# Kernel optimization log

Measured on AMD Instinct MI355X. Metric: run time of the kernel, lower is better.

The kernel has to match this reference:

```python
import jax, jax.numpy as jnp
import numpy as np

HEADS, DIM_HEAD, LANDMARKS, PINV_ITERS, CONV_K = 8, 64, 256, 6, 33


def iter_pinv(x, iters=PINV_ITERS):
    # Moore-Penrose iterative pseudo-inverse (lucidrains nystrom_attention)
    abs_x = jnp.abs(x)
    scale = abs_x.sum(-1).max() * abs_x.sum(-2).max()  # global maxes, as in torch.max
    z = jnp.swapaxes(x, -1, -2) / scale
    I = jnp.eye(x.shape[-1], dtype=x.dtype)
    for _ in range(iters):
        xz = x @ z
        z = 0.25 * z @ (13.0 * I - xz @ (15.0 * I - xz @ (7.0 * I - xz)))
    return z


def nystrom_attention(h, W_qkv, W_out, b_out, conv_w):
    b, n, _ = h.shape
    inner = HEADS * DIM_HEAD
    qkv = h @ W_qkv  # (b, n, 3*inner), bias=False
    q, k, v = jnp.split(qkv, 3, axis=-1)
    split_heads = lambda t: t.reshape(b, n, HEADS, DIM_HEAD).transpose(0, 2, 1, 3)
    q, k, v = split_heads(q), split_heads(k), split_heads(v)  # (b,h,n,dh)
    q = q * (DIM_HEAD ** -0.5)
    l = n // LANDMARKS  # tokens per landmark (n divisible by m, so no padding)
    q_l = q.reshape(b, HEADS, LANDMARKS, l, DIM_HEAD).mean(3)
    k_l = k.reshape(b, HEADS, LANDMARKS, l, DIM_HEAD).mean(3)
    sim1 = jnp.einsum('bhnd,bhmd->bhnm', q, k_l)      # (b,h,n,m)
    sim2 = jnp.einsum('bhmd,bhld->bhml', q_l, k_l)    # (b,h,m,m)
    sim3 = jnp.einsum('bhmd,bhnd->bhmn', q_l, k)      # (b,h,m,n)
    attn1 = jax.nn.softmax(sim1, -1)
    attn2 = jax.nn.softmax(sim2, -1)
    attn3 = jax.nn.softmax(sim3, -1)
    out = (attn1 @ iter_pinv(attn2)) @ (attn3 @ v)    # (b,h,n,dh)
    # residual depthwise conv along sequence dim: Conv2d(heads, heads, (33,1), groups=heads, no bias)
    res = jax.lax.conv_general_dilated(
        v, conv_w, window_strides=(1, 1),
        padding=((CONV_K // 2, CONV_K // 2), (0, 0)),
        feature_group_count=HEADS)
    out = out + res
    out = out.transpose(0, 2, 1, 3).reshape(b, n, inner)
    return out @ W_out + b_out


def setup_inputs() -> dict:
    key = jax.random.key(0)
    ks = jax.random.split(key, 8)
    N, Din, Dout = 8192, 1024, 256
    inner = HEADS * DIM_HEAD
    s = 0.02
    return {
        'x': jax.random.normal(ks[0], (1, N, Din), jnp.float32),
        'W_ft': jax.random.normal(ks[1], (Din, Dout), jnp.float32) * s,
        'b_ft': jnp.zeros((Dout,), jnp.float32),
        'W_qkv': jax.random.normal(ks[2], (Dout, 3 * inner), jnp.float32) * s,
        'W_out': jax.random.normal(ks[3], (inner, Dout), jnp.float32) * s,
        'b_out': jnp.zeros((Dout,), jnp.float32),
        'conv_w': jax.random.normal(ks[4], (HEADS, 1, CONV_K, 1), jnp.float32) * s,
        'W_score': jax.random.normal(ks[5], (Dout, 1), jnp.float32) * s,
        'b_score': jnp.zeros((1,), jnp.float32),
    }


def reference(x, W_ft, b_ft, W_qkv, W_out, b_out, conv_w, W_score, b_score):
    # feature_transform: Linear -> Dropout (identity in eval) -> ReLU
    h = jax.nn.relu(x @ W_ft + b_ft)                 # (1, N, Dout)
    af = nystrom_attention(h, W_qkv, W_out, b_out, conv_w)
    # score_layer: Linear -> Dropout -> ReLU
    scores = jax.nn.relu(af @ W_score + b_score)     # (1, N, 1)
    scores = scores[0].T                             # (1, N)
    weights = jax.nn.softmax(scores, axis=1)         # (1, N)
    aggregated = weights @ h[0]                      # (1, Dout)
    return aggregated, weights
```

## Files before the change

### kernel.cpp

```cpp
#include <hip/hip_runtime.h>

typedef unsigned short u16;
typedef __attribute__((ext_vector_type(8))) short s16x8;
typedef __attribute__((ext_vector_type(4))) float f32x4;
typedef __attribute__((ext_vector_type(8))) unsigned short u16x8;

__device__ inline float b2f(u16 u) {
  unsigned x = ((unsigned)u) << 16;
  return __builtin_bit_cast(float, x);
}
__device__ inline u16 f2b(float f) {
  unsigned u = __builtin_bit_cast(unsigned, f);
  u += 0x7fffu + ((u >> 16) & 1u);
  return (u16)(u >> 16);
}

#define GLL(src, dst) __builtin_amdgcn_global_load_lds( \
    (const __attribute__((address_space(1))) unsigned int*)(src), \
    (__attribute__((address_space(3))) unsigned int*)(dst), 16, 0, 0)

struct MP {
  const u16* A; const u16* B;
  u16* C; u16* Ct; float* Cf; u16* vTo;
  const u16* Aadd; const float* bias;
  const float* Ws; float* sc;
  int M, N, K;
  int lda, ldb, ldc, ldct, ldcf, ldaadd;
  long long bA, bB, bC, bCt, bCf, bAadd;
  float alpha, beta;
  int relu, scale_cols; float colscale;
  int kchunks;
};

template<int BM, int BN, bool F32A>
__global__ __launch_bounds__(256) void gemm_mfma(MP p)
{
  constexpr int WM = BM / 2, WN = BN / 2;
  constexpr int FM = WM / 16, FN = WN / 16;
  constexpr int APAN = BM / 16, BPAN = BN / 16, NPAN = APAN + BPAN;
  constexpr int APW = (APAN + 3) / 4;
  __shared__ __align__(16) u16 lds[2 * NPAN * 512];

  const int tid = threadIdx.x, lane = tid & 63, wid = tid >> 6;
  const int bz = blockIdx.z;
  const int batch = (p.kchunks > 1) ? bz / p.kchunks : bz;
  const int kc    = (p.kchunks > 1) ? bz % p.kchunks : 0;
  const u16* A = p.A + (long long)batch * p.bA + (long long)kc * p.K;
  const float* Af32 = (const float*)p.A + (long long)batch * p.bA + (long long)kc * p.K;
  const u16* B = p.B + (long long)batch * p.bB + (long long)kc * p.K;
  const int m0 = blockIdx.y * BM, n0 = blockIdx.x * BN;
  const int srow = lane & 15, skoff = (lane >> 4) * 8;
  const int wm0 = (wid >> 1) * WM, wn0 = (wid & 1) * WN;

  f32x4 acc[FM][FN];
#pragma unroll
  for (int i = 0; i < FM; i++)
#pragma unroll
    for (int j = 0; j < FN; j++) acc[i][j] = (f32x4){0.f, 0.f, 0.f, 0.f};

  float4 areg[APW][2];

  auto stage_all = [&](int sb, int kt) {
#pragma unroll
    for (int pp = wid; pp < NPAN; pp += 4) {
      const u16* src = (pp < APAN)
        ? A + (size_t)(m0 + pp * 16 + srow) * p.lda + kt + skoff
        : B + (size_t)(n0 + (pp - APAN) * 16 + srow) * p.ldb + kt + skoff;
      GLL(src, &lds[sb * (NPAN * 512) + pp * 512]);
    }
  };
  auto stage_b = [&](int sb, int kt) {
#pragma unroll
    for (int pp = APAN + wid; pp < NPAN; pp += 4) {
      const u16* src = B + (size_t)(n0 + (pp - APAN) * 16 + srow) * p.ldb + kt + skoff;
      GLL(src, &lds[sb * (NPAN * 512) + pp * 512]);
    }
  };
  auto load_a = [&](int kt) {
#pragma unroll
    for (int ap = 0; ap < APW; ap++) {
      int pp = wid + ap * 4;
      const float* src = Af32 + (size_t)(m0 + pp * 16 + srow) * p.lda + kt + skoff;
      areg[ap][0] = ((const float4*)src)[0];
      areg[ap][1] = ((const float4*)src)[1];
    }
  };
  auto write_a = [&](int sb) {
#pragma unroll
    for (int ap = 0; ap < APW; ap++) {
      int pp = wid + ap * 4;
      u16 t[8];
      t[0] = f2b(areg[ap][0].x); t[1] = f2b(areg[ap][0].y);
      t[2] = f2b(areg[ap][0].z); t[3] = f2b(areg[ap][0].w);
      t[4] = f2b(areg[ap][1].x); t[5] = f2b(areg[ap][1].y);
      t[6] = f2b(areg[ap][1].z); t[7] = f2b(areg[ap][1].w);
      *(s16x8*)&lds[sb * (NPAN * 512) + pp * 512 + lane * 8] = *(const s16x8*)t;
    }
  };
  auto compute = [&](int sb) {
    const int bo = sb * (NPAN * 512);
    s16x8 afr[FM], bfr[FN];
#pragma unroll
    for (int i = 0; i < FM; i++)
      afr[i] = *(const s16x8*)&lds[bo + (wm0 / 16 + i) * 512 + lane * 8];
#pragma unroll
    for (int j = 0; j < FN; j++)
      bfr[j] = *(const s16x8*)&lds[bo + (APAN + wn0 / 16 + j) * 512 + lane * 8];
#pragma unroll
    for (int i = 0; i < FM; i++)
#pragma unroll
      for (int j = 0; j < FN; j++)
        acc[i][j] = __builtin_amdgcn_mfma_f32_16x16x32_bf16(afr[i], bfr[j], acc[i][j], 0, 0, 0);
  };

  const int nt = p.K / 32;
  int buf = 0;
  if constexpr (F32A) { load_a(0); stage_b(0, 0); write_a(0); }
  else                { stage_all(0, 0); }
  asm volatile("s_waitcnt vmcnt(0)" ::: "memory");
  __syncthreads();

  for (int t = 0; t < nt; ++t) {
    if constexpr (F32A) {
      if (t + 1 < nt) { load_a((t + 1) * 32); stage_b(buf ^ 1, (t + 1) * 32); }
      compute(buf);
      if (t + 1 < nt) write_a(buf ^ 1);
    } else {
      if (t + 1 < nt) stage_all(buf ^ 1, (t + 1) * 32);
      compute(buf);
    }
    asm volatile("s_waitcnt vmcnt(0)" ::: "memory");
    __syncthreads();
    buf ^= 1;
  }

  const int r0 = (lane >> 4) * 4, c0 = lane & 15;

  if (p.Ws) {
    float* sb = (float*)lds;
#pragma unroll
    for (int i = 0; i < FM; i++)
#pragma unroll
      for (int q = 0; q < 4; q++) {
        float s = 0.f;
#pragma unroll
        for (int j = 0; j < FN; j++)
          s += acc[i][j][q] * p.Ws[wn0 + j * 16 + c0];
        s += __shfl_xor(s, 1); s += __shfl_xor(s, 2);
        s += __shfl_xor(s, 4); s += __shfl_xor(s, 8);
        if ((lane & 15) == 0) sb[(wid & 1) * 64 + wm0 + i * 16 + r0 + q] = s;
      }
    __syncthreads();
    if (tid < 64)
      p.sc[(size_t)bz * 8192 + m0 + tid] = sb[tid] + sb[64 + tid];
    return;
  }

#pragma unroll
  for (int i = 0; i < FM; i++) {
#pragma unroll
    for (int j = 0; j < FN; j++) {
#pragma unroll
      for (int q = 0; q < 4; q++) {
        const int gr = m0 + wm0 + i * 16 + r0 + q;
        const int gc = n0 + wn0 + j * 16 + c0;
        float c = p.alpha * acc[i][j][q];
        if (p.Aadd) c += p.beta * b2f(p.Aadd[(long long)batch * p.bAadd + (size_t)gr * p.ldaadd + gc]);
        if (p.bias) c += p.bias[gc];
        if (gc < p.scale_cols) c *= p.colscale;
        if (p.relu) c = fmaxf(c, 0.f);
        if (p.Cf) p.Cf[(long long)bz * p.bCf + (size_t)gr * p.ldcf + gc] = c;
        u16 b = f2b(c);
        if (p.C)  p.C [(long long)batch * p.bC + (size_t)gr * p.ldc + gc] = b;
        if (p.Ct) p.Ct[(long long)batch * p.bCt + (size_t)gc * p.ldct + gr] = b;
        if (p.vTo && gc >= 1024) p.vTo[(size_t)(gc - 1024) * 8192 + gr] = b;
      }
    }
  }
}

__global__ void reduce_bias_bf16(const float* __restrict__ parts,
                                 const float* __restrict__ bias,
                                 u16* __restrict__ out)
{
  const int i4 = blockIdx.x * 256 + threadIdx.x;
  float4 s = ((const float4*)parts)[i4];
#pragma unroll
  for (int k = 1; k < 4; k++) {
    float4 v = ((const float4*)parts)[(size_t)k * 524288 + i4];
    s.x += v.x; s.y += v.y; s.z += v.z; s.w += v.w;
  }
  const float4 b = ((const float4*)bias)[i4 & 63];
  s.x = fmaxf(s.x + b.x, 0.f); s.y = fmaxf(s.y + b.y, 0.f);
  s.z = fmaxf(s.z + b.z, 0.f); s.w = fmaxf(s.w + b.w, 0.f);
  ushort4 o; o.x = f2b(s.x); o.y = f2b(s.y); o.z = f2b(s.z); o.w = f2b(s.w);
  ((ushort4*)out)[i4] = o;
}

struct AVF { const u16 *qkvb, *ql, *vT; float *Cf, *den; };

__global__ __launch_bounds__(256) void av_fused(AVF p)
{
  __shared__ __align__(16) u16 lds[20480];
  const int tid = threadIdx.x, lane = tid & 63, wid = tid >> 6;
  const int bz = blockIdx.z, head = bz >> 4, kc = bz & 15;
  const int m0 = blockIdx.y * 128;
  const int srow = lane & 15, skoff = (lane >> 4) * 8;
  const int r0 = (lane >> 4) * 4, c0 = lane & 15;
  const u16* Kb = p.qkvb + 512 + (size_t)(kc * 512) * 1536 + head * 64;
  const u16* Vb = p.vT + (size_t)head * 524288 + kc * 512;
  const u16* QL = p.ql + head * 16384 + (size_t)m0 * 64;

#pragma unroll
  for (int q = 0; q < 4; q++) {
    int pid = wid * 4 + q, pr = pid >> 1, kc2 = pid & 1;
    GLL(QL + (size_t)(pr * 16 + srow) * 64 + kc2 * 32 + skoff, &lds[pid * 512]);
  }
  auto stage_kv = [&](int sb, int t) {
    int kr = wid >> 1, kc2 = wid & 1;
    GLL(Kb + (size_t)(t * 32 + kr * 16 + srow) * 1536 + kc2 * 32 + skoff,
        &lds[8192 + sb * 2048 + wid * 512]);
    GLL(Vb + (size_t)(wid * 16 + srow) * 8192 + t * 32 + skoff,
        &lds[12288 + sb * 2048 + wid * 512]);
  };

  f32x4 acc[4][2];
#pragma unroll
  for (int i = 0; i < 4; i++)
#pragma unroll
    for (int j = 0; j < 2; j++) acc[i][j] = (f32x4){0.f, 0.f, 0.f, 0.f};
  float den[2][4];
#pragma unroll
  for (int i = 0; i < 2; i++)
#pragma unroll
    for (int q = 0; q < 4; q++) den[i][q] = 0.f;

  const int nt = 16;
  int buf = 0;
  stage_kv(0, 0);
  asm volatile("s_waitcnt vmcnt(0)" ::: "memory");
  __syncthreads();

  for (int t = 0; t < nt; ++t) {
    if (t + 1 < nt) stage_kv(buf ^ 1, t + 1);
    f32x4 s[2][2];
#pragma unroll
    for (int i = 0; i < 2; i++)
#pragma unroll
      for (int j = 0; j < 2; j++) s[i][j] = (f32x4){0.f, 0.f, 0.f, 0.f};
#pragma unroll
    for (int t2 = 0; t2 < 2; t2++) {
      s16x8 aq[2], bk[2];
#pragma unroll
      for (int i = 0; i < 2; i++)
        aq[i] = *(const s16x8*)&lds[((wid * 2 + i) * 2 + t2) * 512 + lane * 8];
#pragma unroll
      for (int j = 0; j < 2; j++)
        bk[j] = *(const s16x8*)&lds[8192 + buf * 2048 + (j * 2 + t2) * 512 + lane * 8];
#pragma unroll
      for (int i = 0; i < 2; i++)
#pragma unroll
        for (int j = 0; j < 2; j++)
          s[i][j] = __builtin_amdgcn_mfma_f32_16x16x32_bf16(aq[i], bk[j], s[i][j], 0, 0, 0);
    }
#pragma unroll
    for (int i = 0; i < 2; i++)
#pragma unroll
      for (int j = 0; j < 2; j++)
#pragma unroll
        for (int q = 0; q < 4; q++) {
          float e = expf(s[i][j][q]);
          den[i][q] += e;
          int kk = j * 16 + c0;
          lds[16384 + (wid * 2 + i) * 512 + (r0 + q) * 8 + (kk >> 3) * 128 + (kk & 7)] = f2b(e);
        }
    asm volatile("s_waitcnt vmcnt(0)" ::: "memory");
    __syncthreads();
    {
      s16x8 afr[4], bfr[2];
#pragma unroll
      for (int i = 0; i < 4; i++)
        afr[i] = *(const s16x8*)&lds[16384 + ((wid >> 1) * 4 + i) * 512 + lane * 8];
#pragma unroll
      for (int j = 0; j < 2; j++)
        bfr[j] = *(const s16x8*)&lds[12288 + buf * 2048 + ((wid & 1) * 2 + j) * 512 + lane * 8];
#pragma unroll
      for (int i = 0; i < 4; i++)
#pragma unroll
        for (int j = 0; j < 2; j++)
          acc[i][j] = __builtin_amdgcn_mfma_f32_16x16x32_bf16(afr[i], bfr[j], acc[i][j], 0, 0, 0);
    }
    __syncthreads();
    buf ^= 1;
  }

#pragma unroll
  for (int i = 0; i < 4; i++)
#pragma unroll
    for (int j = 0; j < 2; j++)
#pragma unroll
      for (int q = 0; q < 4; q++) {
        const int gr = m0 + (wid >> 1) * 64 + i * 16 + r0 + q;
        const int gc = (wid & 1) * 32 + j * 16 + c0;
        p.Cf[(size_t)bz * 16384 + (size_t)gr * 64 + gc] = acc[i][j][q];
      }
#pragma unroll
  for (int i = 0; i < 2; i++)
#pragma unroll
    for (int q = 0; q < 4; q++) {
      float v = den[i][q];
      v += __shfl_xor(v, 1); v += __shfl_xor(v, 2);
      v += __shfl_xor(v, 4); v += __shfl_xor(v, 8);
      if (c0 == 0)
        p.den[(size_t)bz * 256 + m0 + wid * 32 + i * 16 + r0 + q] = v;
    }
}

struct FA1 { const u16 *qkvb, *kl, *MmT; u16 *af; };

__global__ __launch_bounds__(256) void fused_attn1(FA1 p)
{
  __shared__ __align__(16) u16 lds[36864];
  __shared__ float mb[4][64];
  const int tid = threadIdx.x, lane = tid & 63, wid = tid >> 6;
  const int head = blockIdx.y, n0 = blockIdx.x * 64;
  const int srow = lane & 15, skoff = (lane >> 4) * 8;
  const int rbase = (lane >> 4) * 4;

  for (int pid = wid; pid < 72; pid += 4) {
    const u16* src;
    if (pid < 8) {
      int pr = pid >> 1, kc = pid & 1;
      src = p.qkvb + (size_t)(n0 + pr * 16 + srow) * 1536 + head * 64 + kc * 32 + skoff;
    } else if (pid < 40) {
      int j = pid - 8, pr = j >> 1, kc = j & 1;
      src = p.kl + head * 16384 + (size_t)(pr * 16 + srow) * 64 + kc * 32 + skoff;
    } else {
      int j = pid - 40, pr = j >> 3, kc = j & 7;
      src = p.MmT + head * 16384 + (size_t)(pr * 16 + srow) * 256 + kc * 32 + skoff;
    }
    GLL(src, &lds[pid * 512]);
  }
  asm volatile("s_waitcnt vmcnt(0)" ::: "memory");
  __syncthreads();

  const int wr = (wid >> 1) * 32, ch_ = wid & 1;
  f32x4 s[2][8];
#pragma unroll
  for (int i = 0; i < 2; i++)
#pragma unroll
    for (int j = 0; j < 8; j++) s[i][j] = (f32x4){0.f, 0.f, 0.f, 0.f};
#pragma unroll
  for (int t = 0; t < 2; t++) {
    s16x8 a[2], b[8];
#pragma unroll
    for (int i = 0; i < 2; i++)
      a[i] = *(const s16x8*)&lds[(((wid >> 1) * 2 + i) * 2 + t) * 512 + lane * 8];
#pragma unroll
    for (int j = 0; j < 8; j++)
      b[j] = *(const s16x8*)&lds[4096 + ((ch_ * 8 + j) * 2 + t) * 512 + lane * 8];
#pragma unroll
    for (int i = 0; i < 2; i++)
#pragma unroll
      for (int j = 0; j < 8; j++)
        s[i][j] = __builtin_amdgcn_mfma_f32_16x16x32_bf16(a[i], b[j], s[i][j], 0, 0, 0);
  }
#pragma unroll
  for (int i = 0; i < 2; i++)
#pragma unroll
    for (int q = 0; q < 4; q++) {
      float rm = -INFINITY;
#pragma unroll
      for (int j = 0; j < 8; j++) rm = fmaxf(rm, s[i][j][q]);
#pragma unroll
      for (int off = 1; off < 16; off <<= 1) rm = fmaxf(rm, __shfl_xor(rm, off));
      if ((lane & 15) == 0) mb[ch_][wr + i * 16 + rbase + q] = rm;
    }
  __syncthreads();
  float m_[2][4];
#pragma unroll
  for (int i = 0; i < 2; i++)
#pragma unroll
    for (int q = 0; q < 4; q++)
      m_[i][q] = fmaxf(mb[0][wr + i * 16 + rbase + q], mb[1][wr + i * 16 + rbase + q]);
#pragma unroll
  for (int i = 0; i < 2; i++)
#pragma unroll
    for (int q = 0; q < 4; q++) {
      float ss = 0.f;
#pragma unroll
      for (int j = 0; j < 8; j++) {
        float e = expf(s[i][j][q] - m_[i][q]);
        s[i][j][q] = e; ss += e;
      }
#pragma unroll
      for (int off = 1; off < 16; off <<= 1) ss += __shfl_xor(ss, off);
      if ((lane & 15) == 0) mb[2 + ch_][wr + i * 16 + rbase + q] = ss;
    }
  __syncthreads();
#pragma unroll
  for (int i = 0; i < 2; i++)
#pragma unroll
    for (int q = 0; q < 4; q++) {
      int row = wr + i * 16 + rbase + q;
      float inv = 1.f / (mb[2][row] + mb[3][row]);
#pragma unroll
      for (int j = 0; j < 8; j++)
        lds[(size_t)row * 264 + ch_ * 128 + j * 16 + (lane & 15)] = f2b(s[i][j][q] * inv);
    }
  __syncthreads();
  const int wr2 = (wid >> 1) * 32, wd2 = (wid & 1) * 32;
  f32x4 acc[2][2];
#pragma unroll
  for (int i = 0; i < 2; i++)
#pragma unroll
    for (int jd = 0; jd < 2; jd++) acc[i][jd] = (f32x4){0.f, 0.f, 0.f, 0.f};
#pragma unroll
  for (int t = 0; t < 8; t++) {
    s16x8 a[2], b[2];
#pragma unroll
    for (int i = 0; i < 2; i++)
      a[i] = *(const s16x8*)&lds[(size_t)(wr2 + i * 16 + (lane & 15)) * 264 + t * 32 + (lane >> 4) * 8];
#pragma unroll
    for (int jd = 0; jd < 2; jd++)
      b[jd] = *(const s16x8*)&lds[20480 + (((wid & 1) * 2 + jd) * 8 + t) * 512 + lane * 8];
#pragma unroll
    for (int i = 0; i < 2; i++)
#pragma unroll
      for (int jd = 0; jd < 2; jd++)
        acc[i][jd] = __builtin_amdgcn_mfma_f32_16x16x32_bf16(a[i], b[jd], acc[i][jd], 0, 0, 0);
  }
#pragma unroll
  for (int i = 0; i < 2; i++)
#pragma unroll
    for (int jd = 0; jd < 2; jd++)
#pragma unroll
      for (int q = 0; q < 4; q++)
        p.af[(size_t)(n0 + wr2 + i * 16 + rbase + q) * 512 + head * 64 + wd2 + jd * 16 + (lane & 15)]
            = f2b(acc[i][jd][q]);
}

__global__ void conv_res_add_bf16(const u16* __restrict__ qkvb,
                                  const float* __restrict__ convw,
                                  u16* __restrict__ af)
{
  __shared__ float vt[96][64];
  const int h = blockIdx.y, n0 = blockIdx.x * 64;
  const int t = threadIdx.x, ch = t & 63, r0 = t >> 6;
  for (int r = r0; r < 96; r += 4) {
    int n = n0 - 16 + r;
    float v = 0.f;
    if (n >= 0 && n < 8192) v = b2f(qkvb[(size_t)n * 1536 + 1024 + h * 64 + ch]);
    vt[r][ch] = v;
  }
  __syncthreads();
  float w[33];
#pragma unroll
  for (int j = 0; j < 33; j++) w[j] = convw[h * 33 + j];
  for (int tl = r0; tl < 64; tl += 4) {
    float acc = 0.f;
#pragma unroll
    for (int j = 0; j < 33; j++) acc += w[j] * vt[tl + j][ch];
    size_t o = (size_t)(n0 + tl) * 512 + h * 64 + ch;
    af[o] = f2b(b2f(af[o]) + acc);
  }
}

__global__ void fused_tail(const float* __restrict__ sp,
                           const float* __restrict__ wconst,
                           const u16* __restrict__ hb, float* __restrict__ out)
{
  __shared__ float red[256];
  const int t = threadIdx.x, c = blockIdx.x;
  const float wc = wconst[0];
  float e[32];
  float m = -INFINITY;
#pragma unroll
  for (int i = 0; i < 32; i++) {
    int idx = t + i * 256;
    float v = sp[idx] + sp[8192 + idx] + sp[16384 + idx] + sp[24576 + idx] + wc;
    v = fmaxf(v, 0.f);
    e[i] = v; m = fmaxf(m, v);
  }
  red[t] = m; __syncthreads();
  for (int s = 128; s; s >>= 1) { if (t < s) red[t] = fmaxf(red[t], red[t + s]); __syncthreads(); }
  m = red[0]; __syncthreads();
  float ls = 0.f;
#pragma unroll
  for (int i = 0; i < 32; i++) { e[i] = expf(e[i] - m); ls += e[i]; }
  red[t] = ls; __syncthreads();
  for (int s = 128; s; s >>= 1) { if (t < s) red[t] += red[t + s]; __syncthreads(); }
  const float inv = 1.f / red[0];
  __syncthreads();

  if (c < 256) {
    float acc = 0.f;
#pragma unroll
    for (int i = 0; i < 32; i++)
      acc += e[i] * inv * b2f(hb[(size_t)(t + i * 256) * 256 + c]);
    red[t] = acc; __syncthreads();
    for (int s = 128; s; s >>= 1) { if (t < s) red[t] += red[t + s]; __syncthreads(); }
    if (t == 0) out[c] = red[0];
  } else {
#pragma unroll
    for (int i = 0; i < 32; i++) out[256 + t + i * 256] = e[i] * inv;
  }
}

__global__ void prescale(const u16* __restrict__ x2, float* __restrict__ sbuf)
{
  const int h = blockIdx.x, t = threadIdx.x;
  const u16* X = x2 + ((size_t)h << 16);
  float cs = 0.f;
  for (int r = 0; r < 256; r++) cs += fabsf(b2f(X[r * 256 + t]));
  float rs = 0.f;
  for (int c4 = 0; c4 < 256; c4 += 4) {
    ushort4 v = *(const ushort4*)(X + (size_t)t * 256 + c4);
    rs += fabsf(b2f(v.x)) + fabsf(b2f(v.y)) + fabsf(b2f(v.z)) + fabsf(b2f(v.w));
  }
  __shared__ float red[512];
  red[t] = rs; red[256 + t] = cs;
  __syncthreads();
  for (int s = 128; s; s >>= 1) {
    if (t < s) {
      red[t] = fmaxf(red[t], red[t + s]);
      red[256 + t] = fmaxf(red[256 + t], red[256 + t + s]);
    }
    __syncthreads();
  }
  if (t == 0) { sbuf[h] = red[0]; sbuf[8 + h] = red[256]; }
}

__global__ void pinv_init(const u16* __restrict__ x2, const float* __restrict__ sbuf,
                          u16* __restrict__ z0, u16* __restrict__ z0T)
{
  __shared__ u16 tile[64][80];
  const int t = threadIdx.x;
  const size_t base = (size_t)blockIdx.y << 16;
  const int tr = (blockIdx.x >> 2) * 64, tc = (blockIdx.x & 3) * 64;
  const u16* X = x2 + base;

  float mr = -INFINITY, mc = -INFINITY;
#pragma unroll
  for (int i = 0; i < 8; i++) {
    mr = fmaxf(mr, sbuf[i]);
    mc = fmaxf(mc, sbuf[8 + i]);
  }
  const float inv = 1.f / (mr * mc);

  {
    int r = t >> 2, cg = (t & 3) * 16;
#pragma unroll
    for (int v4 = 0; v4 < 4; v4++) {
      ushort4 v = *(const ushort4*)(X + (size_t)(tr + r) * 256 + tc + cg + v4 * 4);
      v.x = f2b(b2f(v.x) * inv); v.y = f2b(b2f(v.y) * inv);
      v.z = f2b(b2f(v.z) * inv); v.w = f2b(b2f(v.w) * inv);
      *(ushort4*)(z0T + base + (size_t)(tr + r) * 256 + tc + cg + v4 * 4) = v;
      *(ushort4*)&tile[r][cg + v4 * 4] = v;
    }
  }
  __syncthreads();
  {
    int c = t >> 2, rg = (t & 3) * 16;
    u16 o[16];
#pragma unroll
    for (int e = 0; e < 16; e++) o[e] = tile[rg + e][c];
#pragma unroll
    for (int v4 = 0; v4 < 4; v4++)
      *(ushort4*)(z0 + base + (size_t)(tc + c) * 256 + tr + rg + v4 * 4) = *(ushort4*)&o[v4 * 4];
  }
}

struct PG {
  const u16 *U, *V, *Xadd, *XaddT;
  u16 *DR, *DT;
  float alpha, beta;
};

template<bool WD, bool WDT>
__global__ __launch_bounds__(256) void pinv_gemm(PG p)
{
  __shared__ __align__(16) u16 lds[65536 / 2];
  const int tid = threadIdx.x, lane = tid & 63, wid = tid >> 6;
  const size_t base = (size_t)blockIdx.z << 16;
  const u16* U = p.U + base;
  const u16* V = p.V + base;
  const int m0 = blockIdx.y * 64, n0 = blockIdx.x * 64;
  const int srow = lane & 15, skoff = (lane >> 4) * 8;
  const int wr = (wid >> 1) * 32, wc = (wid & 1) * 32;

#pragma unroll
  for (int q = 0; q < 16; q++) {
    const int pid = wid * 16 + q;
    const int rg = (pid >> 3) & 3, t = pid & 7;
    const u16* src = (pid < 32)
      ? U + (size_t)(m0 + rg * 16 + srow) * 256 + t * 32 + skoff
      : V + (size_t)(n0 + rg * 16 + srow) * 256 + t * 32 + skoff;
    GLL(src, &lds[pid * 512]);
  }
  asm volatile("s_waitcnt vmcnt(0)" ::: "memory");
  __syncthreads();

  f32x4 acc[2][2], accT[2][2];
#pragma unroll
  for (int i = 0; i < 2; i++)
#pragma unroll
    for (int j = 0; j < 2; j++) {
      acc[i][j] = (f32x4){0.f, 0.f, 0.f, 0.f};
      accT[i][j] = (f32x4){0.f, 0.f, 0.f, 0.f};
    }

#pragma unroll
  for (int t = 0; t < 8; t++) {
    s16x8 afr[2], bfr[2];
#pragma unroll
    for (int i = 0; i < 2; i++)
      afr[i] = *(const s16x8*)&lds[((wr / 16 + i) * 8 + t) * 512 + lane * 8];
#pragma unroll
    for (int j = 0; j < 2; j++)
      bfr[j] = *(const s16x8*)&lds[(32 + (wc / 16 + j) * 8 + t) * 512 + lane * 8];
#pragma unroll
    for (int i = 0; i < 2; i++)
#pragma unroll
      for (int j = 0; j < 2; j++) {
        if constexpr (WD)
          acc[i][j] = __builtin_amdgcn_mfma_f32_16x16x32_bf16(afr[i], bfr[j], acc[i][j], 0, 0, 0);
        if constexpr (WDT)
          accT[j][i] = __builtin_amdgcn_mfma_f32_16x16x32_bf16(bfr[j], afr[i], accT[j][i], 0, 0, 0);
      }
  }

  const int r0 = (lane >> 4) * 4, c0 = lane & 15;
  if constexpr (WD) {
    const u16* Xa = p.Xadd ? p.Xadd + base : nullptr;
    u16* DR = p.DR + base;
#pragma unroll
    for (int i = 0; i < 2; i++)
#pragma unroll
      for (int j = 0; j < 2; j++)
#pragma unroll
        for (int q = 0; q < 4; q++) {
          const int gr = m0 + wr + i * 16 + r0 + q;
          const int gc = n0 + wc + j * 16 + c0;
          float v = p.alpha * acc[i][j][q];
          if (Xa) v += p.beta * b2f(Xa[(size_t)gr * 256 + gc]);
          DR[(size_t)gr * 256 + gc] = f2b(v);
        }
  }
  if constexpr (WDT) {
    const u16* Xt = p.XaddT ? p.XaddT + base : nullptr;
    u16* DT = p.DT + base;
#pragma unroll
    for (int j = 0; j < 2; j++)
#pragma unroll
      for (int i = 0; i < 2; i++)
#pragma unroll
        for (int q = 0; q < 4; q++) {
          const int gn = n0 + wc + j * 16 + r0 + q;
          const int gm = m0 + wr + i * 16 + c0;
          float v = p.alpha * accT[j][i][q];
          if (Xt) v += p.beta * b2f(Xt[(size_t)gn * 256 + gm]);
          DT[(size_t)gn * 256 + gm] = f2b(v);
        }
  }
}

struct PR1 { const u16 *A, *At, *z; u16 *B, *Bt, *G, *Gt, *W; };

__global__ __launch_bounds__(256) void pinv_r1(PR1 p)
{
  __shared__ __align__(16) u16 lds[32768];
  const int tid = threadIdx.x, lane = tid & 63, wid = tid >> 6;
  const int prob = blockIdx.z >> 3;
  const size_t base = (size_t)(blockIdx.z & 7) << 16;
  const u16* U = (prob ? p.z : p.A) + base;
  const u16* V = p.At + base;
  const int m0 = blockIdx.y * 64, n0 = blockIdx.x * 64;
  const int srow = lane & 15, skoff = (lane >> 4) * 8;
  const int wr = (wid >> 1) * 32, wc = (wid & 1) * 32;

#pragma unroll
  for (int q = 0; q < 16; q++) {
    const int pid = wid * 16 + q;
    const int rg = (pid >> 3) & 3, t = pid & 7;
    const u16* src = (pid < 32)
      ? U + (size_t)(m0 + rg * 16 + srow) * 256 + t * 32 + skoff
      : V + (size_t)(n0 + rg * 16 + srow) * 256 + t * 32 + skoff;
    GLL(src, &lds[pid * 512]);
  }
  asm volatile("s_waitcnt vmcnt(0)" ::: "memory");
  __syncthreads();

  f32x4 acc[2][2], accT[2][2];
#pragma unroll
  for (int i = 0; i < 2; i++)
#pragma unroll
    for (int j = 0; j < 2; j++) {
      acc[i][j] = (f32x4){0.f, 0.f, 0.f, 0.f};
      accT[i][j] = (f32x4){0.f, 0.f, 0.f, 0.f};
    }

#pragma unroll
  for (int t = 0; t < 8; t++) {
    s16x8 afr[2], bfr[2];
#pragma unroll
    for (int i = 0; i < 2; i++)
      afr[i] = *(const s16x8*)&lds[((wr / 16 + i) * 8 + t) * 512 + lane * 8];
#pragma unroll
    for (int j = 0; j < 2; j++)
      bfr[j] = *(const s16x8*)&lds[(32 + (wc / 16 + j) * 8 + t) * 512 + lane * 8];
#pragma unroll
    for (int i = 0; i < 2; i++)
#pragma unroll
      for (int j = 0; j < 2; j++) {
        acc[i][j] = __builtin_amdgcn_mfma_f32_16x16x32_bf16(afr[i], bfr[j], acc[i][j], 0, 0, 0);
        if (prob == 0)
          accT[j][i] = __builtin_amdgcn_mfma_f32_16x16x32_bf16(bfr[j], afr[i], accT[j][i], 0, 0, 0);
      }
  }

  const int r0 = (lane >> 4) * 4, c0 = lane & 15;
  if (prob == 0) {
    const u16* Ab  = p.A  + base;
    const u16* Atb = p.At + base;
    u16 *Bv = p.B + base, *Btv = p.Bt + base;
    u16 *Gv = p.G + base, *Gtv = p.Gt + base;
#pragma unroll
    for (int i = 0; i < 2; i++)
#pragma unroll
      for (int j = 0; j < 2; j++)
#pragma unroll
        for (int q = 0; q < 4; q++) {
          const int gr = m0 + wr + i * 16 + r0 + q;
          const int gc = n0 + wc + j * 16 + c0;
          float b = acc[i][j][q];
          float a = b2f(Ab[(size_t)gr * 256 + gc]);
          Bv[(size_t)gr * 256 + gc] = f2b(b);
          Gv[(size_t)gr * 256 + gc] = f2b(7.f * a - b);
        }
#pragma unroll
    for (int j = 0; j < 2; j++)
#pragma unroll
      for (int i = 0; i < 2; i++)
#pragma unroll
        for (int q = 0; q < 4; q++) {
          const int gn = n0 + wc + j * 16 + r0 + q;
          const int gm = m0 + wr + i * 16 + c0;
          float bt = accT[j][i][q];
          float at = b2f(Atb[(size_t)gn * 256 + gm]);
          Btv[(size_t)gn * 256 + gm] = f2b(bt);
          Gtv[(size_t)gn * 256 + gm] = f2b(7.f * at - bt);
        }
  } else {
    u16* Wv = p.W + base;
#pragma unroll
    for (int i = 0; i < 2; i++)
#pragma unroll
      for (int j = 0; j < 2; j++)
#pragma unroll
        for (int q = 0; q < 4; q++) {
          const int gr = m0 + wr + i * 16 + r0 + q;
          const int gc = n0 + wc + j * 16 + c0;
          Wv[(size_t)gr * 256 + gc] = f2b(acc[i][j][q]);
        }
  }
}

struct PR2 { const u16 *W, *G, *Gt, *B, *Bt, *z, *A, *At; u16 *zo, *Ao, *Aot; };

__global__ __launch_bounds__(256) void pinv_r2(PR2 p)
{
  __shared__ __align__(16) u16 lds[32768];
  const int tid = threadIdx.x, lane = tid & 63, wid = tid >> 6;
  const int prob = blockIdx.z >> 3;
  const size_t base = (size_t)(blockIdx.z & 7) << 16;
  const u16* U = (prob ? p.G  : p.W ) + base;
  const u16* V = (prob ? p.Bt : p.Gt) + base;
  const int m0 = blockIdx.y * 64, n0 = blockIdx.x * 64;
  const int srow = lane & 15, skoff = (lane >> 4) * 8;
  const int wr = (wid >> 1) * 32, wc = (wid & 1) * 32;

#pragma unroll
  for (int q = 0; q < 16; q++) {
    const int pid = wid * 16 + q;
    const int rg = (pid >> 3) & 3, t = pid & 7;
    const u16* src = (pid < 32)
      ? U + (size_t)(m0 + rg * 16 + srow) * 256 + t * 32 + skoff
      : V + (size_t)(n0 + rg * 16 + srow) * 256 + t * 32 + skoff;
    GLL(src, &lds[pid * 512]);
  }
  asm volatile("s_waitcnt vmcnt(0)" ::: "memory");
  __syncthreads();

  f32x4 acc[2][2], accT[2][2];
#pragma unroll
  for (int i = 0; i < 2; i++)
#pragma unroll
    for (int j = 0; j < 2; j++) {
      acc[i][j] = (f32x4){0.f, 0.f, 0.f, 0.f};
      accT[i][j] = (f32x4){0.f, 0.f, 0.f, 0.f};
    }

#pragma unroll
  for (int t = 0; t < 8; t++) {
    s16x8 afr[2], bfr[2];
#pragma unroll
    for (int i = 0; i < 2; i++)
      afr[i] = *(const s16x8*)&lds[((wr / 16 + i) * 8 + t) * 512 + lane * 8];
#pragma unroll
    for (int j = 0; j < 2; j++)
      bfr[j] = *(const s16x8*)&lds[(32 + (wc / 16 + j) * 8 + t) * 512 + lane * 8];
#pragma unroll
    for (int i = 0; i < 2; i++)
#pragma unroll
      for (int j = 0; j < 2; j++) {
        acc[i][j] = __builtin_amdgcn_mfma_f32_16x16x32_bf16(afr[i], bfr[j], acc[i][j], 0, 0, 0);
        if (prob)
          accT[j][i] = __builtin_amdgcn_mfma_f32_16x16x32_bf16(bfr[j], afr[i], accT[j][i], 0, 0, 0);
      }
  }

  const int r0 = (lane >> 4) * 4, c0 = lane & 15;
  if (prob == 0) {
    const u16* Zb = p.z + base;
    const u16* Wb = p.W + base;
    u16* Zo = p.zo + base;
#pragma unroll
    for (int i = 0; i < 2; i++)
#pragma unroll
      for (int j = 0; j < 2; j++)
#pragma unroll
        for (int q = 0; q < 4; q++) {
          const int gr = m0 + wr + i * 16 + r0 + q;
          const int gc = n0 + wc + j * 16 + c0;
          float v = 0.25f * acc[i][j][q]
                  + 3.25f * b2f(Zb[(size_t)gr * 256 + gc])
                  - 3.75f * b2f(Wb[(size_t)gr * 256 + gc]);
          Zo[(size_t)gr * 256 + gc] = f2b(v);
        }
  } else {
    const u16* Ab  = p.A  + base;
    const u16* Bb  = p.B  + base;
    const u16* Atb = p.At + base;
    const u16* Btb = p.Bt + base;
    u16* Ao  = p.Ao  + base;
    u16* Aot = p.Aot + base;
#pragma unroll
    for (int i = 0; i < 2; i++)
#pragma unroll
      for (int j = 0; j < 2; j++)
#pragma unroll
        for (int q = 0; q < 4; q++) {
          const int gr = m0 + wr + i * 16 + r0 + q;
          const int gc = n0 + wc + j * 16 + c0;
          float v = 0.25f * acc[i][j][q]
                  + 3.25f * b2f(Ab[(size_t)gr * 256 + gc])
                  - 3.75f * b2f(Bb[(size_t)gr * 256 + gc]);
          Ao[(size_t)gr * 256 + gc] = f2b(v);
        }
#pragma unroll
    for (int j = 0; j < 2; j++)
#pragma unroll
      for (int i = 0; i < 2; i++)
#pragma unroll
        for (int q = 0; q < 4; q++) {
          const int gn = n0 + wc + j * 16 + r0 + q;
          const int gm = m0 + wr + i * 16 + c0;
          float v = 0.25f * accT[j][i][q]
                  + 3.25f * b2f(Atb[(size_t)gn * 256 + gm])
                  - 3.75f * b2f(Btb[(size_t)gn * 256 + gm]);
          Aot[(size_t)gn * 256 + gm] = f2b(v);
        }
  }
}

__global__ void prep_weights(const float* __restrict__ Wft, const float* __restrict__ Wqkv,
                             const float* __restrict__ Wout, u16* __restrict__ WftT,
                             u16* __restrict__ WqkvT, u16* __restrict__ WoutT,
                             const float* __restrict__ bout, const float* __restrict__ Wsc,
                             const float* __restrict__ bsc, float* __restrict__ wconst)
{
  int idx = blockIdx.x * 256 + threadIdx.x;
  if (blockIdx.x == 0 && threadIdx.x < 64) {
    int c = threadIdx.x * 4;
    float s = bout[c] * Wsc[c] + bout[c + 1] * Wsc[c + 1]
            + bout[c + 2] * Wsc[c + 2] + bout[c + 3] * Wsc[c + 3];
    for (int off = 1; off < 64; off <<= 1) s += __shfl_xor(s, off);
    if (threadIdx.x == 0) wconst[0] = s + bsc[0];
  }
  if (idx < 262144) {
    int r = idx & 1023, c = idx >> 10;
    WftT[idx] = f2b(Wft[(size_t)r * 256 + c]);
  } else if (idx < 655360) {
    int i = idx - 262144;
    int r = i & 255, c = i >> 8;
    WqkvT[i] = f2b(Wqkv[(size_t)r * 1536 + c]);
  } else {
    int i = idx - 655360;
    int r = i & 511, c = i >> 9;
    WoutT[i] = f2b(Wout[(size_t)r * 256 + c]);
  }
}

__global__ void landmark_means(const u16* __restrict__ qkvb,
                               u16* __restrict__ ql, u16* __restrict__ kl)
{
  int idx = blockIdx.x * 256 + threadIdx.x;
  int which = idx >> 17, r = idx & 131071;
  int h = r >> 14, m = (r >> 6) & 255, d = r & 63;
  const u16* src = qkvb + (which ? 512 : 0) + h * 64 + d;
  float s = 0.f; int n0 = m * 32;
  for (int i = 0; i < 32; i++) s += b2f(src[(size_t)(n0 + i) * 1536]);
  (which ? kl : ql)[r] = f2b(s * (1.f / 32.f));
}

__global__ void softmax_rows_bf16_256(u16* __restrict__ d)
{
  const int row = blockIdx.x * 4 + (threadIdx.x >> 6);
  const int lane = threadIdx.x & 63;
  ushort4* p = (ushort4*)(d + (size_t)row * 256);
  ushort4 raw = p[lane];
  float v0 = b2f(raw.x), v1 = b2f(raw.y), v2 = b2f(raw.z), v3 = b2f(raw.w);
  float mx = fmaxf(fmaxf(v0, v1), fmaxf(v2, v3));
  for (int off = 1; off < 64; off <<= 1) mx = fmaxf(mx, __shfl_xor(mx, off));
  v0 = expf(v0 - mx); v1 = expf(v1 - mx); v2 = expf(v2 - mx); v3 = expf(v3 - mx);
  float s = v0 + v1 + v2 + v3;
  for (int off = 1; off < 64; off <<= 1) s += __shfl_xor(s, off);
  float inv = 1.f / s;
  raw.x = f2b(v0 * inv); raw.y = f2b(v1 * inv); raw.z = f2b(v2 * inv); raw.w = f2b(v3 * inv);
  p[lane] = raw;
}

__global__ void reduce_avT(const float* __restrict__ avp, const float* __restrict__ den,
                           u16* __restrict__ avT)
{
  int idx = blockIdx.x * 256 + threadIdx.x;
  int m = idx & 255, d = (idx >> 8) & 63, h = idx >> 14;
  float s = 0.f, l = 0.f;
  for (int c = 0; c < 16; c++) {
    s += avp[((size_t)(h * 16 + c)) * 16384 + m * 64 + d];
    l += den[(size_t)(h * 16 + c) * 256 + m];
  }
  avT[((size_t)h * 64 + d) * 256 + m] = f2b(s / l);
}

extern "C" void kernel_launch(void* const* d_in, const int* in_sizes, int n_in,
                              void* d_out, int out_size, void* d_ws, size_t ws_size,
                              hipStream_t stream)
{
  const float* x       = (const float*)d_in[0];
  const float* W_ft    = (const float*)d_in[1];
  const float* b_ft    = (const float*)d_in[2];
  const float* W_qkv   = (const float*)d_in[3];
  const float* W_out   = (const float*)d_in[4];
  const float* b_out   = (const float*)d_in[5];
  const float* conv_w  = (const float*)d_in[6];
  const float* W_score = (const float*)d_in[7];
  const float* b_score = (const float*)d_in[8];
  float* out = (float*)d_out;

  char* W = (char*)d_ws;
  auto alloc = [&](size_t bytes) { char* r = W; W += (bytes + 255) & ~(size_t)255; return r; };
  u16* WftT  = (u16*)alloc(256ull * 1024 * 2);
  u16* WqkvT = (u16*)alloc(1536ull * 256 * 2);
  u16* WoutT = (u16*)alloc(256ull * 512 * 2);
  u16* hb    = (u16*)alloc(8192ull * 256 * 2);
  u16* qkvb  = (u16*)alloc(8192ull * 1536 * 2);
  u16* ql    = (u16*)alloc(8ull * 256 * 64 * 2);
  u16* kl    = (u16*)alloc(8ull * 256 * 64 * 2);
  u16* x2    = (u16*)alloc(8ull * 256 * 256 * 2);
  u16* z0    = (u16*)alloc(8ull * 256 * 256 * 2);
  u16* z0T   = (u16*)alloc(8ull * 256 * 256 * 2);
  u16* zp    = (u16*)alloc(8ull * 256 * 256 * 2);
  u16* Amat  = (u16*)alloc(8ull * 256 * 256 * 2);
  u16* AmatT = (u16*)alloc(8ull * 256 * 256 * 2);
  u16* Am2   = (u16*)alloc(8ull * 256 * 256 * 2);
  u16* Am2T  = (u16*)alloc(8ull * 256 * 256 * 2);
  u16* Bm    = (u16*)alloc(8ull * 256 * 256 * 2);
  u16* BmT   = (u16*)alloc(8ull * 256 * 256 * 2);
  u16* Gm    = (u16*)alloc(8ull * 256 * 256 * 2);
  u16* GmT   = (u16*)alloc(8ull * 256 * 256 * 2);
  u16* Wm    = (u16*)alloc(8ull * 256 * 256 * 2);
  u16* vT    = (u16*)alloc(8ull * 64 * 8192 * 2);
  float* avp = (float*)alloc(8ull * 16 * 256 * 64 * 4);
  float* denp = (float*)alloc(128ull * 256 * 4);
  u16* avT   = (u16*)alloc(8ull * 64 * 256 * 2);
  u16* MmT   = (u16*)alloc(8ull * 64 * 256 * 2);
  u16* af    = (u16*)alloc(8192ull * 512 * 2);
  float* gpart = (float*)alloc(4ull * 8192 * 256 * 4);
  float* sbuf   = (float*)alloc(256);
  float* scores = (float*)alloc(4ull * 8192 * 4);
  float* wconst = (float*)alloc(256);

  auto mp = [](const u16* A, const u16* B, int M, int N, int K,
               int lda, int ldb, long long bA, long long bB) {
    MP p{}; p.A = A; p.B = B; p.M = M; p.N = N; p.K = K;
    p.lda = lda; p.ldb = ldb; p.bA = bA; p.bB = bB;
    p.alpha = 1.f; p.beta = 0.f; p.kchunks = 1; return p;
  };

  prep_weights<<<3072, 256, 0, stream>>>(W_ft, W_qkv, W_out, WftT, WqkvT, WoutT,
                                         b_out, W_score, b_score, wconst);

  { MP p = mp((const u16*)x, WftT, 8192, 256, 256, 1024, 1024, 0, 0);
    p.kchunks = 4; p.Cf = gpart; p.ldcf = 256; p.bCf = 2097152;
    gemm_mfma<64, 256, true><<<dim3(1, 128, 4), 256, 0, stream>>>(p); }
  reduce_bias_bf16<<<2048, 256, 0, stream>>>(gpart, b_ft, hb);

  { MP p = mp(hb, WqkvT, 8192, 1536, 256, 256, 256, 0, 0);
    p.C = qkvb; p.ldc = 1536; p.scale_cols = 512; p.colscale = 0.125f; p.vTo = vT;
    gemm_mfma<128, 128, false><<<dim3(12, 64, 1), 256, 0, stream>>>(p); }

  landmark_means<<<1024, 256, 0, stream>>>(qkvb, ql, kl);

  { MP p = mp(ql, kl, 256, 256, 64, 64, 64, 16384, 16384);
    p.C = x2; p.ldc = 256; p.bC = 65536;
    gemm_mfma<64, 64, false><<<dim3(4, 4, 8), 256, 0, stream>>>(p); }
  softmax_rows_bf16_256<<<512, 256, 0, stream>>>(x2);

  prescale<<<8, 256, 0, stream>>>(x2, sbuf);
  pinv_init<<<dim3(16, 8), 256, 0, stream>>>(x2, sbuf, z0, z0T);
  { PG p{x2, z0T, nullptr, nullptr, Amat, AmatT, 1.f, 0.f};
    pinv_gemm<true, true><<<dim3(4, 4, 8), 256, 0, stream>>>(p); }
  {
    const dim3 b(256);
    u16 *zr = z0, *zo = zp;
    u16 *Ar = Amat, *Art = AmatT, *Ao = Am2, *Aot = Am2T;
    for (int it = 0; it < 6; it++) {
      { PR1 r{Ar, Art, zr, Bm, BmT, Gm, GmT, Wm};
        pinv_r1<<<dim3(4, 4, 16), b, 0, stream>>>(r); }
      { PR2 r{Wm, Gm, GmT, Bm, BmT, zr, Ar, Art, zo, Ao, Aot};
        pinv_r2<<<dim3(4, 4, (it == 5) ? 8 : 16), b, 0, stream>>>(r); }
      u16* t;
      t = zr; zr = zo; zo = t;
      t = Ar; Ar = Ao; Ao = t;
      t = Art; Art = Aot; Aot = t;
    }
  }

  { AVF p{qkvb, ql, vT, avp, denp};
    av_fused<<<dim3(1, 2, 128), 256, 0, stream>>>(p); }
  reduce_avT<<<512, 256, 0, stream>>>(avp, denp, avT);

  { MP p = mp(z0, avT, 256, 64, 256, 256, 256, 65536, 16384);
    p.Ct = MmT; p.ldct = 256; p.bCt = 16384;
    gemm_mfma<64, 64, false><<<dim3(1, 4, 8), 256, 0, stream>>>(p); }

  { FA1 fp{qkvb, kl, MmT, af};
    fused_attn1<<<dim3(128, 8), 256, 0, stream>>>(fp); }

  conv_res_add_bf16<<<dim3(128, 8), 256, 0, stream>>>(qkvb, conv_w, af);

  { MP p = mp(af, WoutT, 8192, 256, 128, 512, 512, 0, 0);
    p.kchunks = 4; p.Ws = W_score; p.sc = scores;
    gemm_mfma<64, 256, false><<<dim3(1, 128, 4), 256, 0, stream>>>(p); }

  fused_tail<<<257, 256, 0, stream>>>(scores, wconst, hb, out);
}
```

Before: 331.3 us.

## Fuse conv residual into attn1 epilogue, split av_fused finer, parallelize prescale

The depthwise conv residual is now computed inside fused_attn1's epilogue. It restages a 96-row V window into LDS and adds it before the single bf16 store, removing one kernel launch and the read-modify-write of af. av_fused splits the sequence into 32 chunks instead of 16, doubling the grid for occupancy, with a longer partial reduction to match. prescale uses 16 blocks, separating row and column sums to add parallelism. Costs are extra LDS reuse and syncs in attn1 and more partial-buffer traffic.

```diff
diff --git a/kernel.cpp b/kernel.cpp
--- a/kernel.cpp
+++ b/kernel.cpp
@@ -203,12 +203,12 @@
 {
   __shared__ __align__(16) u16 lds[20480];
   const int tid = threadIdx.x, lane = tid & 63, wid = tid >> 6;
-  const int bz = blockIdx.z, head = bz >> 4, kc = bz & 15;
+  const int bz = blockIdx.z, head = bz >> 5, kc = bz & 31;
   const int m0 = blockIdx.y * 128;
   const int srow = lane & 15, skoff = (lane >> 4) * 8;
   const int r0 = (lane >> 4) * 4, c0 = lane & 15;
-  const u16* Kb = p.qkvb + 512 + (size_t)(kc * 512) * 1536 + head * 64;
-  const u16* Vb = p.vT + (size_t)head * 524288 + kc * 512;
+  const u16* Kb = p.qkvb + 512 + (size_t)(kc * 256) * 1536 + head * 64;
+  const u16* Vb = p.vT + (size_t)head * 524288 + kc * 256;
   const u16* QL = p.ql + head * 16384 + (size_t)m0 * 64;
 
 #pragma unroll
@@ -235,7 +235,7 @@
 #pragma unroll
     for (int q = 0; q < 4; q++) den[i][q] = 0.f;
 
-  const int nt = 16;
+  const int nt = 8;
   int buf = 0;
   stage_kv(0, 0);
   asm volatile("s_waitcnt vmcnt(0)" ::: "memory");
@@ -316,7 +316,7 @@
     }
 }
 
-struct FA1 { const u16 *qkvb, *kl, *MmT; u16 *af; };
+struct FA1 { const u16 *qkvb, *kl, *MmT; const float* convw; u16 *af; };
 
 __global__ __launch_bounds__(256) void fused_attn1(FA1 p)
 {
@@ -430,40 +430,36 @@
       for (int jd = 0; jd < 2; jd++)
         acc[i][jd] = __builtin_amdgcn_mfma_f32_16x16x32_bf16(a[i], b[jd], acc[i][jd], 0, 0, 0);
   }
+
+  __syncthreads();
+  {
+    float* wb = &mb[0][0];
+    if (tid < 33) wb[tid] = p.convw[head * 33 + tid];
+    const int ch = tid & 63, rr0 = tid >> 6;
+    for (int r = rr0; r < 96; r += 4) {
+      int n = n0 - 16 + r;
+      u16 v = 0;
+      if (n >= 0 && n < 8192) v = p.qkvb[(size_t)n * 1536 + 1024 + head * 64 + ch];
+      lds[r * 64 + ch] = v;
+    }
+  }
+  __syncthreads();
+  const float* wb = &mb[0][0];
+
 #pragma unroll
   for (int i = 0; i < 2; i++)
 #pragma unroll
     for (int jd = 0; jd < 2; jd++)
 #pragma unroll
-      for (int q = 0; q < 4; q++)
-        p.af[(size_t)(n0 + wr2 + i * 16 + rbase + q) * 512 + head * 64 + wd2 + jd * 16 + (lane & 15)]
-            = f2b(acc[i][jd][q]);
-}
-
-__global__ void conv_res_add_bf16(const u16* __restrict__ qkvb,
-                                  const float* __restrict__ convw,
-                                  u16* __restrict__ af)
-{
-  __shared__ float vt[96][64];
-  const int h = blockIdx.y, n0 = blockIdx.x * 64;
-  const int t = threadIdx.x, ch = t & 63, r0 = t >> 6;
-  for (int r = r0; r < 96; r += 4) {
-    int n = n0 - 16 + r;
-    float v = 0.f;
-    if (n >= 0 && n < 8192) v = b2f(qkvb[(size_t)n * 1536 + 1024 + h * 64 + ch]);
-    vt[r][ch] = v;
-  }
-  __syncthreads();
-  float w[33];
-#pragma unroll
-  for (int j = 0; j < 33; j++) w[j] = convw[h * 33 + j];
-  for (int tl = r0; tl < 64; tl += 4) {
-    float acc = 0.f;
-#pragma unroll
-    for (int j = 0; j < 33; j++) acc += w[j] * vt[tl + j][ch];
-    size_t o = (size_t)(n0 + tl) * 512 + h * 64 + ch;
-    af[o] = f2b(b2f(af[o]) + acc);
-  }
+      for (int q = 0; q < 4; q++) {
+        const int rl = wr2 + i * 16 + rbase + q;
+        const int d  = wd2 + jd * 16 + (lane & 15);
+        float cv = 0.f;
+#pragma unroll
+        for (int j = 0; j < 33; j++)
+          cv += wb[j] * b2f(lds[(rl + j) * 64 + d]);
+        p.af[(size_t)(n0 + rl) * 512 + head * 64 + d] = f2b(acc[i][jd][q] + cv);
+      }
 }
 
 __global__ void fused_tail(const float* __restrict__ sp,
@@ -509,26 +505,24 @@
 
 __global__ void prescale(const u16* __restrict__ x2, float* __restrict__ sbuf)
 {
-  const int h = blockIdx.x, t = threadIdx.x;
+  const int h = blockIdx.x & 7, which = blockIdx.x >> 3, t = threadIdx.x;
   const u16* X = x2 + ((size_t)h << 16);
-  float cs = 0.f;
-  for (int r = 0; r < 256; r++) cs += fabsf(b2f(X[r * 256 + t]));
-  float rs = 0.f;
-  for (int c4 = 0; c4 < 256; c4 += 4) {
-    ushort4 v = *(const ushort4*)(X + (size_t)t * 256 + c4);
-    rs += fabsf(b2f(v.x)) + fabsf(b2f(v.y)) + fabsf(b2f(v.z)) + fabsf(b2f(v.w));
-  }
-  __shared__ float red[512];
-  red[t] = rs; red[256 + t] = cs;
-  __syncthreads();
-  for (int s = 128; s; s >>= 1) {
-    if (t < s) {
-      red[t] = fmaxf(red[t], red[t + s]);
-      red[256 + t] = fmaxf(red[256 + t], red[256 + t + s]);
-    }
+  __shared__ float red[256];
+  float s = 0.f;
+  if (which == 0) {
+    for (int c4 = 0; c4 < 256; c4 += 4) {
+      ushort4 v = *(const ushort4*)(X + (size_t)t * 256 + c4);
+      s += fabsf(b2f(v.x)) + fabsf(b2f(v.y)) + fabsf(b2f(v.z)) + fabsf(b2f(v.w));
+    }
+  } else {
+    for (int r = 0; r < 256; r++) s += fabsf(b2f(X[r * 256 + t]));
+  }
+  red[t] = s; __syncthreads();
+  for (int st = 128; st; st >>= 1) {
+    if (t < st) red[t] = fmaxf(red[t], red[t + st]);
     __syncthreads();
   }
-  if (t == 0) { sbuf[h] = red[0]; sbuf[8 + h] = red[256]; }
+  if (t == 0) sbuf[which * 8 + h] = red[0];
 }
 
 __global__ void pinv_init(const u16* __restrict__ x2, const float* __restrict__ sbuf,
@@ -937,9 +931,9 @@
   int idx = blockIdx.x * 256 + threadIdx.x;
   int m = idx & 255, d = (idx >> 8) & 63, h = idx >> 14;
   float s = 0.f, l = 0.f;
-  for (int c = 0; c < 16; c++) {
-    s += avp[((size_t)(h * 16 + c)) * 16384 + m * 64 + d];
-    l += den[(size_t)(h * 16 + c) * 256 + m];
+  for (int c = 0; c < 32; c++) {
+    s += avp[((size_t)(h * 32 + c)) * 16384 + m * 64 + d];
+    l += den[(size_t)(h * 32 + c) * 256 + m];
   }
   avT[((size_t)h * 64 + d) * 256 + m] = f2b(s / l);
 }
@@ -982,8 +976,8 @@
   u16* GmT   = (u16*)alloc(8ull * 256 * 256 * 2);
   u16* Wm    = (u16*)alloc(8ull * 256 * 256 * 2);
   u16* vT    = (u16*)alloc(8ull * 64 * 8192 * 2);
-  float* avp = (float*)alloc(8ull * 16 * 256 * 64 * 4);
-  float* denp = (float*)alloc(128ull * 256 * 4);
+  float* avp = (float*)alloc(256ull * 16384 * 4);
+  float* denp = (float*)alloc(256ull * 256 * 4);
   u16* avT   = (u16*)alloc(8ull * 64 * 256 * 2);
   u16* MmT   = (u16*)alloc(8ull * 64 * 256 * 2);
   u16* af    = (u16*)alloc(8192ull * 512 * 2);
@@ -1018,7 +1012,7 @@
     gemm_mfma<64, 64, false><<<dim3(4, 4, 8), 256, 0, stream>>>(p); }
   softmax_rows_bf16_256<<<512, 256, 0, stream>>>(x2);
 
-  prescale<<<8, 256, 0, stream>>>(x2, sbuf);
+  prescale<<<16, 256, 0, stream>>>(x2, sbuf);
   pinv_init<<<dim3(16, 8), 256, 0, stream>>>(x2, sbuf, z0, z0T);
   { PG p{x2, z0T, nullptr, nullptr, Amat, AmatT, 1.f, 0.f};
     pinv_gemm<true, true><<<dim3(4, 4, 8), 256, 0, stream>>>(p); }
@@ -1039,17 +1033,15 @@
   }
 
   { AVF p{qkvb, ql, vT, avp, denp};
-    av_fused<<<dim3(1, 2, 128), 256, 0, stream>>>(p); }
+    av_fused<<<dim3(1, 2, 256), 256, 0, stream>>>(p); }
   reduce_avT<<<512, 256, 0, stream>>>(avp, denp, avT);
 
   { MP p = mp(z0, avT, 256, 64, 256, 256, 256, 65536, 16384);
     p.Ct = MmT; p.ldct = 256; p.bCt = 16384;
     gemm_mfma<64, 64, false><<<dim3(1, 4, 8), 256, 0, stream>>>(p); }
 
-  { FA1 fp{qkvb, kl, MmT, af};
+  { FA1 fp{qkvb, kl, MmT, conv_w, af};
     fused_attn1<<<dim3(128, 8), 256, 0, stream>>>(fp); }
-
-  conv_res_add_bf16<<<dim3(128, 8), 256, 0, stream>>>(qkvb, conv_w, af);
 
   { MP p = mp(af, WoutT, 8192, 256, 128, 512, 512, 0, 0);
     p.kchunks = 4; p.Ws = W_score; p.sc = scores;
```

Result: slower. 349.7 us (+5.6%).
